# Performance work log

Measured on AMD Instinct MI355X. Metric: run time of the kernel, lower is better.

The kernel has to match this reference:

```python
import jax, jax.numpy as jnp
import numpy as np
from jax import lax

STRIDE = 1
PAD = 1


def _unfold(x, k, stride, padding):
    # torch.nn.functional.unfold: patches ordered (c, kh, kw), channel slowest
    N, C, H, W = x.shape
    xp = jnp.pad(x, ((0, 0), (0, 0), (padding, padding), (padding, padding)))
    Ho = (H - k + 2 * padding) // stride + 1
    Wo = (W - k + 2 * padding) // stride + 1
    cols = [xp[:, :, i:i + stride * Ho:stride, j:j + stride * Wo:stride]
            for i in range(k) for j in range(k)]  # k*k slices of (N,C,Ho,Wo)
    p = jnp.stack(cols, axis=2)  # (N, C, k*k, Ho, Wo) -> (c, kh, kw) ordering
    return p.reshape(N, C * k * k, Ho * Wo), Ho, Wo


def setup_inputs() -> dict:
    key = jax.random.key(0)
    k1, k2 = jax.random.split(key)
    x = jax.random.normal(k1, (16, 128, 28, 28), dtype=jnp.float32)
    W = jax.random.normal(k2, (256, 128, 3, 3), dtype=jnp.float32)
    return {"x": x, "W": W}


def reference(x, W):
    O, C, k, _ = W.shape
    N = x.shape[0]
    Xc, Ho, Wo = _unfold(x, k, STRIDE, PAD)          # (N, d, L)
    d = C * k * k
    Xp = Xc.transpose(0, 2, 1).reshape(N * Ho * Wo, d)  # (P, d), P = N*Ho*Wo
    Wf = W.reshape(O, d)                               # (O, d)
    # out[f, p] = -sum_d |W[f,d] - X[p,d]|  (AdderNet: -cdist(W, X, p=1))
    # Stream over filters to avoid the O*P*d pairwise buffer.
    out = -lax.map(lambda w: jnp.sum(jnp.abs(w[None, :] - Xp), axis=-1), Wf)  # (O, P)
    return out.reshape(O, N, Ho, Wo).transpose(1, 0, 2, 3)  # (N, O, Ho, Wo)
```

## Files before the change

### kernel.cpp

```cpp
#include <hip/hip_runtime.h>


typedef unsigned int u32;

#define WD 28
#define HW 784
#define CIN 128
#define OUT_F 256
#define TN 8
#define NW 4
#define C4PW 8
#define WL_N (32 * 9 * TN)
#define SSTR 31
#define SLAB_N (16 * SSTR)
#define S_TOT (WL_N + NW * SLAB_N)

#define QSCALE 23.0f
#define QBIAS  127.0f
#define PADB   0x7F7F7F7Fu

static __device__ __forceinline__ u32 quant4(float a, float b, float c, float d) {
#if __has_builtin(__builtin_amdgcn_cvt_pk_u8_f32)
    u32 p = 0;
    p = __builtin_amdgcn_cvt_pk_u8_f32(fmaf(a, QSCALE, QBIAS), 0, p);
    p = __builtin_amdgcn_cvt_pk_u8_f32(fmaf(b, QSCALE, QBIAS), 1, p);
    p = __builtin_amdgcn_cvt_pk_u8_f32(fmaf(c, QSCALE, QBIAS), 2, p);
    p = __builtin_amdgcn_cvt_pk_u8_f32(fmaf(d, QSCALE, QBIAS), 3, p);
    return p;
#else
    auto q1 = [](float v) -> u32 {
        float t = fmaf(v, QSCALE, QBIAS);
        t = fminf(fmaxf(t, 0.f), 255.f);
        return (u32)(t + 0.5f);
    };
    return q1(a) | (q1(b) << 8) | (q1(c) << 16) | (q1(d) << 24);
#endif
}

static __device__ __forceinline__ u32 sad4(u32 a, u32 b, u32 acc) {
#if __has_builtin(__builtin_amdgcn_sad_u8)
    return __builtin_amdgcn_sad_u8(a, b, acc);
#else
    #pragma unroll
    for (int i = 0; i < 4; ++i) {
        const int av = (a >> (8 * i)) & 0xFF;
        const int bv = (b >> (8 * i)) & 0xFF;
        acc += (u32)((av > bv) ? (av - bv) : (bv - av));
    }
    return acc;
#endif
}

__global__ __launch_bounds__(256, 2) void adder2d_kernel(
    const float* __restrict__ x,
    const float* __restrict__ Wf,
    float* __restrict__ out)
{
    __shared__ __align__(16) u32 S[S_TOT];

    u32* const Wl = S;

    const int tid  = threadIdx.x;
    const int bx   = blockIdx.x;
    const int n    = bx >> 1;
    const int hb   = bx & 1;
    const int h0   = hb * 14;
    const int f0   = blockIdx.y * TN;
    const int wid  = tid >> 6;
    const int lane = tid & 63;
    const int kb   = wid * C4PW;

    u32* const slab = S + WL_N + wid * SLAB_N;

    #pragma unroll
    for (int k = 0; k < 9; ++k) {
        const int m  = tid + k * 256;
        const int ff = m & 7;
        const int q  = m >> 3;
        const int s  = q % 9;
        const int c4 = q / 9;
        const float* b = Wf + ((size_t)(f0 + ff) * CIN + 4 * c4) * 9 + s;
        Wl[m] = quant4(b[0], b[9], b[18], b[27]);
    }
    if (lane < 32) {
        const int r = lane >> 1, sd = lane & 1;
        slab[r * SSTR + (sd ? 29 : 0)] = PADB;
    }

    const float* xn = x + (size_t)n * CIN * HW;
    float lv[4][4];

    #define STAGE(c4g)                                                        \
        {                                                                     \
            const float* xc = xn + (size_t)(4 * (c4g)) * HW;                  \
            _Pragma("unroll")                                                 \
            for (int k = 0; k < 4; ++k) {                                     \
                const int slot = lane + k * 64;                               \
                const int r = slot / 28, w = slot - r * 28;                   \
                const int h = h0 - 1 + r;                                     \
                if (h >= 0 && h < WD) {                                       \
                    const float* p = xc + h * WD + w;                         \
                    lv[k][0] = p[0];      lv[k][1] = p[HW];                   \
                    lv[k][2] = p[2 * HW]; lv[k][3] = p[3 * HW];               \
                }                                                             \
            }                                                                 \
            _Pragma("unroll")                                                 \
            for (int k = 0; k < 4; ++k) {                                     \
                const int slot = lane + k * 64;                               \
                const int r = slot / 28, w = slot - r * 28;                   \
                const int h = h0 - 1 + r;                                     \
                u32 qv = PADB;                                                \
                if (h >= 0 && h < WD)                                         \
                    qv = quant4(lv[k][0], lv[k][1], lv[k][2], lv[k][3]);      \
                slab[r * SSTR + w + 1] = qv;                                  \
            }                                                                 \
            _Pragma("unroll")                                                 \
            for (int k = 4; k < 7; ++k) {                                     \
                const int slot = lane + k * 64;                               \
                const int r = slot / 28, w = slot - r * 28;                   \
                const int h = h0 - 1 + r;                                     \
                if (h >= 0 && h < WD) {                                       \
                    const float* p = xc + h * WD + w;                         \
                    lv[k - 4][0] = p[0];      lv[k - 4][1] = p[HW];           \
                    lv[k - 4][2] = p[2 * HW]; lv[k - 4][3] = p[3 * HW];       \
                }                                                             \
            }                                                                 \
            _Pragma("unroll")                                                 \
            for (int k = 4; k < 7; ++k) {                                     \
                const int slot = lane + k * 64;                               \
                const int r = slot / 28, w = slot - r * 28;                   \
                const int h = h0 - 1 + r;                                     \
                u32 qv = PADB;                                                \
                if (h >= 0 && h < WD)                                         \
                    qv = quant4(lv[k - 4][0], lv[k - 4][1],                   \
                                lv[k - 4][2], lv[k - 4][3]);                  \
                slab[r * SSTR + w + 1] = qv;                                  \
            }                                                                 \
        }

    STAGE(kb);
    __syncthreads();

    const bool active = lane < 56;
    const int row = lane >> 2;
    const int cs  = (lane & 3) * 7;

    u32 acc[7][TN] = {};

    #pragma unroll 1
    for (int l = 0; l < C4PW; ++l) {
        if (active) {
            const u32* sb = &slab[row * SSTR + cs];
            u32 xv[3][9];
            #pragma unroll
            for (int i = 0; i < 3; ++i)
                #pragma unroll
                for (int j = 0; j < 9; ++j)
                    xv[i][j] = sb[i * SSTR + j];
            const uint4* wq = reinterpret_cast<const uint4*>(&Wl[(kb + l) * 72]);
            #pragma unroll
            for (int kh = 0; kh < 3; ++kh) {
                #pragma unroll
                for (int kw = 0; kw < 3; ++kw) {
                    const int s = kh * 3 + kw;
                    const uint4 wa = wq[2 * s];
                    const uint4 wb = wq[2 * s + 1];
                    #pragma unroll
                    for (int pc = 0; pc < 7; ++pc) {
                        const u32 xs = xv[kh][kw + pc];
                        acc[pc][0] = sad4(wa.x, xs, acc[pc][0]);
                        acc[pc][1] = sad4(wa.y, xs, acc[pc][1]);
                        acc[pc][2] = sad4(wa.z, xs, acc[pc][2]);
                        acc[pc][3] = sad4(wa.w, xs, acc[pc][3]);
                        acc[pc][4] = sad4(wb.x, xs, acc[pc][4]);
                        acc[pc][5] = sad4(wb.y, xs, acc[pc][5]);
                        acc[pc][6] = sad4(wb.z, xs, acc[pc][6]);
                        acc[pc][7] = sad4(wb.w, xs, acc[pc][7]);
                    }
                }
            }
        }
        if (l + 1 < C4PW) STAGE(kb + l + 1);
    }
    __syncthreads();

    #define MSTR 23
    u32* scr = S;
    #pragma unroll
    for (int c = 0; c < 3; ++c) {
        const int fb = c * 3;
        const int nf = (c == 2) ? 2 : 3;
        if ((wid & 1) && active) {
            #pragma unroll
            for (int g = 0; g < 3; ++g) if (g < nf)
                #pragma unroll
                for (int pc = 0; pc < 7; ++pc)
                    scr[(wid >> 1) * (64 * MSTR) + lane * MSTR + g * 7 + pc]
                        = acc[pc][fb + g];
        }
        __syncthreads();
        if (!(wid & 1) && active) {
            #pragma unroll
            for (int g = 0; g < 3; ++g) if (g < nf)
                #pragma unroll
                for (int pc = 0; pc < 7; ++pc)
                    acc[pc][fb + g] +=
                        scr[(wid >> 1) * (64 * MSTR) + lane * MSTR + g * 7 + pc];
        }
        __syncthreads();
        if (wid == 2 && active) {
            #pragma unroll
            for (int g = 0; g < 3; ++g) if (g < nf)
                #pragma unroll
                for (int pc = 0; pc < 7; ++pc)
                    scr[lane * MSTR + g * 7 + pc] = acc[pc][fb + g];
        }
        __syncthreads();
        if (wid == 0 && active) {
            #pragma unroll
            for (int g = 0; g < 3; ++g) if (g < nf)
                #pragma unroll
                for (int pc = 0; pc < 7; ++pc)
                    acc[pc][fb + g] += scr[lane * MSTR + g * 7 + pc];
        }
        __syncthreads();
    }

    if (wid == 0 && active) {
        const float sc = -(1.0f / QSCALE);
        const int ho = h0 + row;
        float* ob = out + (size_t)n * OUT_F * HW + ho * WD + cs;
        #pragma unroll
        for (int ff = 0; ff < TN; ++ff) {
            float* o = ob + (size_t)(f0 + ff) * HW;
            #pragma unroll
            for (int pc = 0; pc < 7; ++pc)
                o[pc] = (float)acc[pc][ff] * sc;
        }
    }
}

extern "C" void kernel_launch(void* const* d_in, const int* in_sizes, int n_in,
                              void* d_out, int out_size, void* d_ws, size_t ws_size,
                              hipStream_t stream) {
    const float* x  = (const float*)d_in[0];
    const float* Wf = (const float*)d_in[1];
    float* out = (float*)d_out;

    dim3 grid(32, OUT_F / TN);
    adder2d_kernel<<<grid, dim3(256), 0, stream>>>(x, Wf, out);
}
```

Baseline: 54.68 us.

## Double-buffer per-wave input slabs and prefetch global loads two stages ahead

Each wave now keeps two LDS slabs and alternates between them. Quantized writes of the next channel group and global loads for the group after that are interleaved with the SAD compute, split across kh rows. This is meant to hide global memory latency, which the old code exposed by staging serially after each compute iteration. In exchange it doubles per-wave slab LDS, raises register pressure (lv grows to 7x4 floats held across compute), and relies on wave-local ordering with no barrier between the slab writes and reads.

```diff
diff --git a/kernel.cpp b/kernel.cpp
--- a/kernel.cpp
+++ b/kernel.cpp
@@ -13,7 +13,7 @@
 #define WL_N (32 * 9 * TN)
 #define SSTR 31
 #define SLAB_N (16 * SSTR)
-#define S_TOT (WL_N + NW * SLAB_N)
+#define S_TOT (WL_N + NW * 2 * SLAB_N)
 
 #define QSCALE 23.0f
 #define QBIAS  127.0f
@@ -70,7 +70,8 @@
     const int lane = tid & 63;
     const int kb   = wid * C4PW;
 
-    u32* const slab = S + WL_N + wid * SLAB_N;
+    u32* const slab0 = S + WL_N + wid * (2 * SLAB_N);
+    u32* const slab1 = slab0 + SLAB_N;
 
     #pragma unroll
     for (int k = 0; k < 9; ++k) {
@@ -82,19 +83,20 @@
         const float* b = Wf + ((size_t)(f0 + ff) * CIN + 4 * c4) * 9 + s;
         Wl[m] = quant4(b[0], b[9], b[18], b[27]);
     }
-    if (lane < 32) {
-        const int r = lane >> 1, sd = lane & 1;
-        slab[r * SSTR + (sd ? 29 : 0)] = PADB;
+    {
+        const int bsel = lane >> 5;
+        const int r = (lane >> 1) & 15, sd = lane & 1;
+        (bsel ? slab1 : slab0)[r * SSTR + (sd ? 29 : 0)] = PADB;
     }
 
     const float* xn = x + (size_t)n * CIN * HW;
-    float lv[4][4];
-
-    #define STAGE(c4g)                                                        \
+    float lv[7][4];
+
+    #define LOADX(c4g)                                                        \
         {                                                                     \
             const float* xc = xn + (size_t)(4 * (c4g)) * HW;                  \
             _Pragma("unroll")                                                 \
-            for (int k = 0; k < 4; ++k) {                                     \
+            for (int k = 0; k < 7; ++k) {                                     \
                 const int slot = lane + k * 64;                               \
                 const int r = slot / 28, w = slot - r * 28;                   \
                 const int h = h0 - 1 + r;                                     \
@@ -104,41 +106,25 @@
                     lv[k][2] = p[2 * HW]; lv[k][3] = p[3 * HW];               \
                 }                                                             \
             }                                                                 \
+        }
+
+    #define WRITEX(dst)                                                       \
+        {                                                                     \
             _Pragma("unroll")                                                 \
-            for (int k = 0; k < 4; ++k) {                                     \
+            for (int k = 0; k < 7; ++k) {                                     \
                 const int slot = lane + k * 64;                               \
                 const int r = slot / 28, w = slot - r * 28;                   \
                 const int h = h0 - 1 + r;                                     \
                 u32 qv = PADB;                                                \
                 if (h >= 0 && h < WD)                                         \
                     qv = quant4(lv[k][0], lv[k][1], lv[k][2], lv[k][3]);      \
-                slab[r * SSTR + w + 1] = qv;                                  \
+                (dst)[r * SSTR + w + 1] = qv;                                 \
             }                                                                 \
-            _Pragma("unroll")                                                 \
-            for (int k = 4; k < 7; ++k) {                                     \
-                const int slot = lane + k * 64;                               \
-                const int r = slot / 28, w = slot - r * 28;                   \
-                const int h = h0 - 1 + r;                                     \
-                if (h >= 0 && h < WD) {                                       \
-                    const float* p = xc + h * WD + w;                         \
-                    lv[k - 4][0] = p[0];      lv[k - 4][1] = p[HW];           \
-                    lv[k - 4][2] = p[2 * HW]; lv[k - 4][3] = p[3 * HW];       \
-                }                                                             \
-            }                                                                 \
-            _Pragma("unroll")                                                 \
-            for (int k = 4; k < 7; ++k) {                                     \
-                const int slot = lane + k * 64;                               \
-                const int r = slot / 28, w = slot - r * 28;                   \
-                const int h = h0 - 1 + r;                                     \
-                u32 qv = PADB;                                                \
-                if (h >= 0 && h < WD)                                         \
-                    qv = quant4(lv[k - 4][0], lv[k - 4][1],                   \
-                                lv[k - 4][2], lv[k - 4][3]);                  \
-                slab[r * SSTR + w + 1] = qv;                                  \
-            }                                                                 \
-        }
-
-    STAGE(kb);
+        }
+
+    LOADX(kb);
+    WRITEX(slab0);
+    LOADX(kb + 1);
     __syncthreads();
 
     const bool active = lane < 56;
@@ -149,17 +135,26 @@
 
     #pragma unroll 1
     for (int l = 0; l < C4PW; ++l) {
-        if (active) {
-            const u32* sb = &slab[row * SSTR + cs];
-            u32 xv[3][9];
-            #pragma unroll
-            for (int i = 0; i < 3; ++i)
-                #pragma unroll
-                for (int j = 0; j < 9; ++j)
-                    xv[i][j] = sb[i * SSTR + j];
-            const uint4* wq = reinterpret_cast<const uint4*>(&Wl[(kb + l) * 72]);
-            #pragma unroll
-            for (int kh = 0; kh < 3; ++kh) {
+        u32* const cur = (l & 1) ? slab1 : slab0;
+        u32* const nxt = (l & 1) ? slab0 : slab1;
+        const uint4* wq = reinterpret_cast<const uint4*>(&Wl[(kb + l) * 72]);
+        const u32* sb = cur + row * SSTR + cs;
+
+        u32 xv[9];
+
+        #pragma unroll
+        for (int kh = 0; kh < 3; ++kh) {
+            #pragma unroll
+            for (int j = 0; j < 9; ++j)
+                xv[j] = sb[kh * SSTR + j];
+
+            if (kh == 0) {
+                if (l + 1 < C4PW) WRITEX(nxt);
+            } else if (kh == 1) {
+                if (l + 2 < C4PW) LOADX(kb + l + 2);
+            }
+
+            if (active) {
                 #pragma unroll
                 for (int kw = 0; kw < 3; ++kw) {
                     const int s = kh * 3 + kw;
@@ -167,7 +162,7 @@
                     const uint4 wb = wq[2 * s + 1];
                     #pragma unroll
                     for (int pc = 0; pc < 7; ++pc) {
-                        const u32 xs = xv[kh][kw + pc];
+                        const u32 xs = xv[kw + pc];
                         acc[pc][0] = sad4(wa.x, xs, acc[pc][0]);
                         acc[pc][1] = sad4(wa.y, xs, acc[pc][1]);
                         acc[pc][2] = sad4(wa.z, xs, acc[pc][2]);
@@ -180,7 +175,6 @@
                 }
             }
         }
-        if (l + 1 < C4PW) STAGE(kb + l + 1);
     }
     __syncthreads();
 
```

Result: no change. 54.99 us (+0.6%).
